# Optimization experiments

Hardware: AMD Instinct MI355X
Metric: run time of the kernel (lower is better)

The kernel has to match this reference:

```python
import jax, jax.numpy as jnp
import numpy as np

LECUN_A, LECUN_B = 1.7159, 0.666

def lecun_tanh(x):
    return LECUN_A * jnp.tanh(LECUN_B * x)

def setup_inputs() -> dict:
    key = jax.random.key(0)
    ks = jax.random.split(key, 16)
    B, T, D, H, BB, U, C = 128, 512, 1024, 512, 128, 32, 3
    def p(k, shape, fan_in):
        lim = 1.0 / np.sqrt(fan_in)
        return jax.random.uniform(k, shape, jnp.float32, -lim, lim)
    return {
        "x": jax.random.normal(ks[0], (B, T, D), jnp.float32),
        # vars[0], vars[1]: Linear(1024 -> 512)
        "W0": p(ks[1], (H, D), D), "b0": p(ks[2], (H,), D),
        # self.ltc CfC(512, 32): backbone Linear(512+32 -> 128), then ff1/ff2/time_a/time_b Linear(128 -> 32)
        "Wb": p(ks[3], (BB, H + U), H + U), "bb": p(ks[4], (BB,), H + U),
        "Wff1": p(ks[5], (U, BB), BB), "bff1": p(ks[6], (U,), BB),
        "Wff2": p(ks[7], (U, BB), BB), "bff2": p(ks[8], (U,), BB),
        "Wta": p(ks[9], (U, BB), BB), "bta": p(ks[10], (U,), BB),
        "Wtb": p(ks[11], (U, BB), BB), "btb": p(ks[12], (U,), BB),
        # vars[12], vars[13]: Linear(32 -> 3)
        "W2": p(ks[13], (C, U), U), "b2": p(ks[14], (C,), U),
    }

def reference(x, W0, b0, Wb, bb, Wff1, bff1, Wff2, bff2, Wta, bta, Wtb, btb, W2, b2):
    # x: [B, T, 1024] -> Linear -> GELU (dropout is identity in eval mode)
    h0 = jnp.einsum("btd,hd->bth", x, W0) + b0          # [B, T, 512]
    h0 = jax.nn.gelu(h0, approximate=False)
    B = x.shape[0]
    U = Wff1.shape[0]

    def step(h, xt):
        z = jnp.concatenate([xt, h], axis=-1)           # [B, 544]
        g = lecun_tanh(z @ Wb.T + bb)                   # backbone, [B, 128]
        ff1 = jnp.tanh(g @ Wff1.T + bff1)
        ff2 = jnp.tanh(g @ Wff2.T + bff2)
        t_a = g @ Wta.T + bta
        t_b = g @ Wtb.T + btb
        t_interp = jax.nn.sigmoid(t_a * 1.0 + t_b)      # ts = 1.0 per step
        h_new = ff1 * (1.0 - t_interp) + t_interp * ff2
        return h_new, h_new

    h_init = jnp.zeros((B, U), x.dtype)
    _, seq = jax.lax.scan(step, h_init, jnp.swapaxes(h0, 0, 1))  # [T, B, 32]
    seq = jnp.swapaxes(seq, 0, 1)                                # [B, T, 32]
    y = jax.nn.gelu(seq, approximate=False)
    logits = jnp.einsum("btu,cu->btc", y, W2) + b2               # [B, T, 3]
    pooled = jnp.max(logits, axis=1)                             # [B, 3]
    return jax.nn.softmax(pooled, axis=1)
```

## Files before the change

kernel.cpp:

```cpp
#include <hip/hip_runtime.h>
#include <hip/hip_bf16.h>
#include <cstdint>

typedef __bf16 bf16x8 __attribute__((ext_vector_type(8)));
typedef float  f32x4  __attribute__((ext_vector_type(4)));

__device__ __forceinline__ unsigned short f2bf(float f) {
    union { float f; uint32_t u; } v; v.f = f;
    uint32_t r = (v.u + 0x7FFFu + ((v.u >> 16) & 1u)) >> 16;
    return (unsigned short)r;
}

__device__ __forceinline__ float fast_tanh(float x) {
    x = fminf(10.f, fmaxf(-10.f, x));
    float e = __expf(2.f * x);
    return (e - 1.f) / (e + 1.f);
}

__device__ __forceinline__ float gelu_exact(float x) {
    return 0.5f * x * (1.0f + erff(x * 0.70710678118654752f));
}

__global__ __launch_bounds__(256) void convert_weights_kernel(
    const float* __restrict__ W0, const float* __restrict__ Wb,
    unsigned short* __restrict__ W0bf, unsigned short* __restrict__ Wbxbf)
{
    int i = blockIdx.x * 256 + threadIdx.x;
    if (i < 512 * 1024) W0bf[i] = f2bf(W0[i]);
    if (i < 128 * 512) {
        int n = i >> 9, k = i & 511;
        Wbxbf[i] = f2bf(Wb[n * 544 + k]);
    }
}

template <int NT, bool A_F32, bool GELU_OUT>
__global__ __launch_bounds__(256) void gemm_kernel(
    const void* __restrict__ Aptr, const unsigned short* __restrict__ B,
    const float* __restrict__ bias, void* __restrict__ Cptr,
    int M, int N, int K)
{
    __shared__ alignas(16) unsigned short Als[128 * 32];
    __shared__ alignas(16) unsigned short Bls[128 * 32];

    const int bid = blockIdx.x;
    const int nb = bid & (NT - 1);
    const int mb = bid / NT;
    const int m0 = mb * 128;
    const int n0 = nb * 128;

    const int t = threadIdx.x;
    const int w = t >> 6, l = t & 63;
    const int wr = w >> 1, wc = w & 1;
    const int lr = l & 15, lk = (l >> 4) * 8;

    f32x4 acc[4][4];
    const f32x4 zero = {0.f, 0.f, 0.f, 0.f};
#pragma unroll
    for (int i = 0; i < 4; ++i)
#pragma unroll
        for (int j = 0; j < 4; ++j) acc[i][j] = zero;

    for (int k0 = 0; k0 < K; k0 += 32) {
        if constexpr (A_F32) {
            const float* A = (const float*)Aptr;
#pragma unroll
            for (int p = 0; p < 4; ++p) {
                int r = p * 32 + (t >> 3);
                int kq = (t & 7) * 4;
                float4 v = *reinterpret_cast<const float4*>(
                    &A[(size_t)(m0 + r) * K + k0 + kq]);
                ushort4 o;
                o.x = f2bf(v.x); o.y = f2bf(v.y);
                o.z = f2bf(v.z); o.w = f2bf(v.w);
                *reinterpret_cast<ushort4*>(&Als[r * 32 + kq]) = o;
            }
        } else {
            const unsigned short* A = (const unsigned short*)Aptr;
#pragma unroll
            for (int p = 0; p < 2; ++p) {
                int r = p * 64 + (t >> 2);
                int kq = (t & 3) * 8;
                *reinterpret_cast<uint4*>(&Als[r * 32 + kq]) =
                    *reinterpret_cast<const uint4*>(&A[(size_t)(m0 + r) * K + k0 + kq]);
            }
        }
#pragma unroll
        for (int p = 0; p < 2; ++p) {
            int r = p * 64 + (t >> 2);
            int kq = (t & 3) * 8;
            *reinterpret_cast<uint4*>(&Bls[r * 32 + kq]) =
                *reinterpret_cast<const uint4*>(&B[(size_t)(n0 + r) * K + k0 + kq]);
        }
        __syncthreads();

        bf16x8 af[4], bfr[4];
#pragma unroll
        for (int i = 0; i < 4; ++i)
            af[i] = *reinterpret_cast<const bf16x8*>(&Als[(wr * 64 + i * 16 + lr) * 32 + lk]);
#pragma unroll
        for (int j = 0; j < 4; ++j)
            bfr[j] = *reinterpret_cast<const bf16x8*>(&Bls[(wc * 64 + j * 16 + lr) * 32 + lk]);
#pragma unroll
        for (int i = 0; i < 4; ++i)
#pragma unroll
            for (int j = 0; j < 4; ++j)
                acc[i][j] = __builtin_amdgcn_mfma_f32_16x16x32_bf16(
                    af[i], bfr[j], acc[i][j], 0, 0, 0);
        __syncthreads();
    }

#pragma unroll
    for (int i = 0; i < 4; ++i) {
#pragma unroll
        for (int j = 0; j < 4; ++j) {
            int col = n0 + wc * 64 + j * 16 + (l & 15);
            int rowb = m0 + wr * 64 + i * 16 + (l >> 4) * 4;
            float bv = bias[col];
#pragma unroll
            for (int p = 0; p < 4; ++p) {
                float v = acc[i][j][p] + bv;
                size_t idx = (size_t)(rowb + p) * N + col;
                if constexpr (GELU_OUT) {
                    ((unsigned short*)Cptr)[idx] = f2bf(gelu_exact(v));
                } else {
                    ((float*)Cptr)[idx] = v;
                }
            }
        }
    }
}

__global__ __launch_bounds__(512) void scan_kernel(
    const float* __restrict__ pre_g, const float* __restrict__ Wb,
    const float* __restrict__ Wff1, const float* __restrict__ bff1,
    const float* __restrict__ Wff2, const float* __restrict__ bff2,
    const float* __restrict__ Wta,  const float* __restrict__ bta,
    const float* __restrict__ Wtb,  const float* __restrict__ btb,
    float* __restrict__ seq)
{
    __shared__ alignas(16) float h_lds[32];
    __shared__ alignas(16) float g_lds[144];
    __shared__ alignas(16) float head_lds[128];

    const int tid = threadIdx.x;
    const int b = blockIdx.x;
    const int u = tid >> 2;
    const int q = tid & 3;

    float wbh[8];
#pragma unroll
    for (int j = 0; j < 8; ++j) wbh[j] = Wb[u * 544 + 512 + q * 8 + j];

    const int which = u >> 5;
    const int uu = u & 31;
    const float* Wh = (which == 0) ? Wff1 : (which == 1) ? Wff2 : (which == 2) ? Wta : Wtb;
    const float* bh = (which == 0) ? bff1 : (which == 1) ? bff2 : (which == 2) ? bta : btb;
    float whr[32];
#pragma unroll
    for (int j4 = 0; j4 < 8; ++j4) {
        float4 v = *reinterpret_cast<const float4*>(&Wh[uu * 128 + q * 32 + j4 * 4]);
        whr[j4 * 4 + 0] = v.x; whr[j4 * 4 + 1] = v.y;
        whr[j4 * 4 + 2] = v.z; whr[j4 * 4 + 3] = v.w;
    }
    const float hbias = bh[uu];

    if (tid < 32) h_lds[tid] = 0.0f;
    __syncthreads();

    const size_t base = (size_t)b * 512 * 128;
    const size_t sbase = (size_t)b * 512 * 32;
    float pg0 = pre_g[base + u];
    float pg1 = pre_g[base + 128 + u];

    for (int step = 0; step < 512; ++step) {
        float pg2 = 0.f;
        if (step + 2 < 512) pg2 = pre_g[base + (size_t)(step + 2) * 128 + u];

        float s = 0.f;
#pragma unroll
        for (int j2 = 0; j2 < 2; ++j2) {
            float4 hv = *reinterpret_cast<const float4*>(&h_lds[q * 8 + j2 * 4]);
            s = fmaf(wbh[j2 * 4 + 0], hv.x, s);
            s = fmaf(wbh[j2 * 4 + 1], hv.y, s);
            s = fmaf(wbh[j2 * 4 + 2], hv.z, s);
            s = fmaf(wbh[j2 * 4 + 3], hv.w, s);
        }
        s += __shfl_xor(s, 1);
        s += __shfl_xor(s, 2);
        float g = 1.7159f * fast_tanh(0.666f * (pg0 + s));
        if (q == 0) g_lds[u + ((u >> 5) << 2)] = g;
        __syncthreads();

        float d = 0.f;
        const float* gq = &g_lds[q * 36];
#pragma unroll
        for (int j4 = 0; j4 < 8; ++j4) {
            float4 gv = *reinterpret_cast<const float4*>(&gq[j4 * 4]);
            d = fmaf(whr[j4 * 4 + 0], gv.x, d);
            d = fmaf(whr[j4 * 4 + 1], gv.y, d);
            d = fmaf(whr[j4 * 4 + 2], gv.z, d);
            d = fmaf(whr[j4 * 4 + 3], gv.w, d);
        }
        d += __shfl_xor(d, 1);
        d += __shfl_xor(d, 2);
        d += hbias;
        if (u < 64) d = fast_tanh(d);
        if (q == 0) head_lds[u] = d;
        __syncthreads();

        if (tid < 32) {
            float ff1 = head_lds[tid], ff2 = head_lds[32 + tid];
            float ta = head_lds[64 + tid], tb = head_lds[96 + tid];
            float ti = 1.0f / (1.0f + __expf(-(ta + tb)));
            float hn = ff1 + ti * (ff2 - ff1);
            h_lds[tid] = hn;
            seq[sbase + (size_t)step * 32 + tid] = hn;
        }
        __syncthreads();

        pg0 = pg1; pg1 = pg2;
    }
}

__global__ __launch_bounds__(256) void final_kernel(
    const float* __restrict__ seq, const float* __restrict__ W2,
    const float* __restrict__ b2, float* __restrict__ out)
{
    const int b = blockIdx.x, tid = threadIdx.x;
    __shared__ float w2s[96];
    __shared__ float redbuf[12];
    if (tid < 96) w2s[tid] = W2[tid];
    __syncthreads();

    float m0 = -1e30f, m1 = -1e30f, m2 = -1e30f;
    for (int t = tid; t < 512; t += 256) {
        const float* row = &seq[(size_t)(b * 512 + t) * 32];
        float l0 = 0.f, l1 = 0.f, l2 = 0.f;
#pragma unroll
        for (int u4 = 0; u4 < 8; ++u4) {
            float4 v = *reinterpret_cast<const float4*>(&row[u4 * 4]);
            float xs[4] = {v.x, v.y, v.z, v.w};
#pragma unroll
            for (int e = 0; e < 4; ++e) {
                float y = gelu_exact(xs[e]);
                int uidx = u4 * 4 + e;
                l0 = fmaf(y, w2s[uidx], l0);
                l1 = fmaf(y, w2s[32 + uidx], l1);
                l2 = fmaf(y, w2s[64 + uidx], l2);
            }
        }
        m0 = fmaxf(m0, l0); m1 = fmaxf(m1, l1); m2 = fmaxf(m2, l2);
    }
#pragma unroll
    for (int off = 32; off; off >>= 1) {
        m0 = fmaxf(m0, __shfl_xor(m0, off));
        m1 = fmaxf(m1, __shfl_xor(m1, off));
        m2 = fmaxf(m2, __shfl_xor(m2, off));
    }
    if ((tid & 63) == 0) {
        int wv = tid >> 6;
        redbuf[wv * 3 + 0] = m0; redbuf[wv * 3 + 1] = m1; redbuf[wv * 3 + 2] = m2;
    }
    __syncthreads();
    if (tid == 0) {
        float a0 = -1e30f, a1 = -1e30f, a2 = -1e30f;
        for (int i = 0; i < 4; ++i) {
            a0 = fmaxf(a0, redbuf[i * 3 + 0]);
            a1 = fmaxf(a1, redbuf[i * 3 + 1]);
            a2 = fmaxf(a2, redbuf[i * 3 + 2]);
        }
        a0 += b2[0]; a1 += b2[1]; a2 += b2[2];
        float mm = fmaxf(a0, fmaxf(a1, a2));
        float e0 = expf(a0 - mm), e1 = expf(a1 - mm), e2 = expf(a2 - mm);
        float inv = 1.0f / (e0 + e1 + e2);
        out[b * 3 + 0] = e0 * inv;
        out[b * 3 + 1] = e1 * inv;
        out[b * 3 + 2] = e2 * inv;
    }
}

extern "C" void kernel_launch(void* const* d_in, const int* in_sizes, int n_in,
                              void* d_out, int out_size, void* d_ws, size_t ws_size,
                              hipStream_t stream)
{
    const float* x    = (const float*)d_in[0];
    const float* W0   = (const float*)d_in[1];
    const float* b0   = (const float*)d_in[2];
    const float* Wb   = (const float*)d_in[3];
    const float* bb   = (const float*)d_in[4];
    const float* Wff1 = (const float*)d_in[5];
    const float* bff1 = (const float*)d_in[6];
    const float* Wff2 = (const float*)d_in[7];
    const float* bff2 = (const float*)d_in[8];
    const float* Wta  = (const float*)d_in[9];
    const float* bta  = (const float*)d_in[10];
    const float* Wtb  = (const float*)d_in[11];
    const float* btb  = (const float*)d_in[12];
    const float* W2   = (const float*)d_in[13];
    const float* b2   = (const float*)d_in[14];

    char* ws = (char*)d_ws;
    unsigned short* h0bf  = (unsigned short*)(ws);
    float*          pre_g = (float*)(ws + 67108864);
    float*          seq   = (float*)(ws + 100663296);
    unsigned short* W0bf  = (unsigned short*)(ws + 109051904);
    unsigned short* Wbxbf = (unsigned short*)(ws + 110100480);
    (void)ws_size; (void)in_sizes; (void)n_in; (void)out_size;

    convert_weights_kernel<<<2048, 256, 0, stream>>>(W0, Wb, W0bf, Wbxbf);

    gemm_kernel<4, true, true><<<2048, 256, 0, stream>>>(
        (const void*)x, W0bf, b0, (void*)h0bf, 65536, 512, 1024);

    gemm_kernel<1, false, false><<<512, 256, 0, stream>>>(
        (const void*)h0bf, Wbxbf, bb, (void*)pre_g, 65536, 128, 512);

    scan_kernel<<<128, 512, 0, stream>>>(pre_g, Wb,
        Wff1, bff1, Wff2, bff2, Wta, bta, Wtb, btb, seq);

    final_kernel<<<128, 256, 0, stream>>>(seq, W2, b2, (float*)d_out);
}
```

Baseline: 948.9 us.

## Widen GEMM K-tile, restructure scan to two barriers per step, vectorize conversion

The GEMM K-tile grows from 32 to 64, which halves the number of barrier pairs per output tile at the cost of twice the shared memory. The scan kernel changes its head mapping so the four heads for one unit sit in the same 16 lanes. The gate combination is then done with shuffles, which drops the head_lds buffer and one __syncthreads per step. The scan also prefetches pre_g in chunks of 8 steps and splits its FMA chains into several independent accumulators, and weight conversion now uses float4 loads. The GEMM LDS layout, with a 64-element row stride, may cause more bank conflicts on the fragment reads.

```diff
diff --git a/kernel.cpp b/kernel.cpp
--- a/kernel.cpp
+++ b/kernel.cpp
@@ -26,10 +26,18 @@
     unsigned short* __restrict__ W0bf, unsigned short* __restrict__ Wbxbf)
 {
     int i = blockIdx.x * 256 + threadIdx.x;
-    if (i < 512 * 1024) W0bf[i] = f2bf(W0[i]);
-    if (i < 128 * 512) {
-        int n = i >> 9, k = i & 511;
-        Wbxbf[i] = f2bf(Wb[n * 544 + k]);
+    if (i < 131072) {
+        float4 v = reinterpret_cast<const float4*>(W0)[i];
+        ushort4 o;
+        o.x = f2bf(v.x); o.y = f2bf(v.y); o.z = f2bf(v.z); o.w = f2bf(v.w);
+        reinterpret_cast<ushort4*>(W0bf)[i] = o;
+    }
+    if (i < 16384) {
+        int n = i >> 7, k4 = i & 127;
+        float4 v = *reinterpret_cast<const float4*>(&Wb[n * 544 + k4 * 4]);
+        ushort4 o;
+        o.x = f2bf(v.x); o.y = f2bf(v.y); o.z = f2bf(v.z); o.w = f2bf(v.w);
+        reinterpret_cast<ushort4*>(Wbxbf)[i] = o;
     }
 }
 
@@ -39,8 +47,8 @@
     const float* __restrict__ bias, void* __restrict__ Cptr,
     int M, int N, int K)
 {
-    __shared__ alignas(16) unsigned short Als[128 * 32];
-    __shared__ alignas(16) unsigned short Bls[128 * 32];
+    __shared__ alignas(16) unsigned short Als[128 * 64];
+    __shared__ alignas(16) unsigned short Bls[128 * 64];
 
     const int bid = blockIdx.x;
     const int nb = bid & (NT - 1);
@@ -60,52 +68,57 @@
 #pragma unroll
         for (int j = 0; j < 4; ++j) acc[i][j] = zero;
 
-    for (int k0 = 0; k0 < K; k0 += 32) {
+    for (int k0 = 0; k0 < K; k0 += 64) {
         if constexpr (A_F32) {
             const float* A = (const float*)Aptr;
 #pragma unroll
-            for (int p = 0; p < 4; ++p) {
-                int r = p * 32 + (t >> 3);
-                int kq = (t & 7) * 4;
+            for (int p = 0; p < 8; ++p) {
+                int r = p * 16 + (t >> 4);
+                int kq = (t & 15) * 4;
                 float4 v = *reinterpret_cast<const float4*>(
                     &A[(size_t)(m0 + r) * K + k0 + kq]);
                 ushort4 o;
                 o.x = f2bf(v.x); o.y = f2bf(v.y);
                 o.z = f2bf(v.z); o.w = f2bf(v.w);
-                *reinterpret_cast<ushort4*>(&Als[r * 32 + kq]) = o;
+                *reinterpret_cast<ushort4*>(&Als[r * 64 + kq]) = o;
             }
         } else {
             const unsigned short* A = (const unsigned short*)Aptr;
 #pragma unroll
-            for (int p = 0; p < 2; ++p) {
-                int r = p * 64 + (t >> 2);
-                int kq = (t & 3) * 8;
-                *reinterpret_cast<uint4*>(&Als[r * 32 + kq]) =
-                    *reinterpret_cast<const uint4*>(&A[(size_t)(m0 + r) * K + k0 + kq]);
-            }
-        }
-#pragma unroll
-        for (int p = 0; p < 2; ++p) {
-            int r = p * 64 + (t >> 2);
-            int kq = (t & 3) * 8;
-            *reinterpret_cast<uint4*>(&Bls[r * 32 + kq]) =
-                *reinterpret_cast<const uint4*>(&B[(size_t)(n0 + r) * K + k0 + kq]);
+            for (int p = 0; p < 4; ++p) {
+                int idx = p * 256 + t;
+                int r = idx >> 3, c = (idx & 7) * 8;
+                *reinterpret_cast<uint4*>(&Als[r * 64 + c]) =
+                    *reinterpret_cast<const uint4*>(&A[(size_t)(m0 + r) * K + k0 + c]);
+            }
+        }
+#pragma unroll
+        for (int p = 0; p < 4; ++p) {
+            int idx = p * 256 + t;
+            int r = idx >> 3, c = (idx & 7) * 8;
+            *reinterpret_cast<uint4*>(&Bls[r * 64 + c]) =
+                *reinterpret_cast<const uint4*>(&B[(size_t)(n0 + r) * K + k0 + c]);
         }
         __syncthreads();
 
-        bf16x8 af[4], bfr[4];
-#pragma unroll
-        for (int i = 0; i < 4; ++i)
-            af[i] = *reinterpret_cast<const bf16x8*>(&Als[(wr * 64 + i * 16 + lr) * 32 + lk]);
-#pragma unroll
-        for (int j = 0; j < 4; ++j)
-            bfr[j] = *reinterpret_cast<const bf16x8*>(&Bls[(wc * 64 + j * 16 + lr) * 32 + lk]);
-#pragma unroll
-        for (int i = 0; i < 4; ++i)
+#pragma unroll
+        for (int kk = 0; kk < 64; kk += 32) {
+            bf16x8 af[4], bfr[4];
+#pragma unroll
+            for (int i = 0; i < 4; ++i)
+                af[i] = *reinterpret_cast<const bf16x8*>(
+                    &Als[(wr * 64 + i * 16 + lr) * 64 + kk + lk]);
 #pragma unroll
             for (int j = 0; j < 4; ++j)
-                acc[i][j] = __builtin_amdgcn_mfma_f32_16x16x32_bf16(
-                    af[i], bfr[j], acc[i][j], 0, 0, 0);
+                bfr[j] = *reinterpret_cast<const bf16x8*>(
+                    &Bls[(wc * 64 + j * 16 + lr) * 64 + kk + lk]);
+#pragma unroll
+            for (int i = 0; i < 4; ++i)
+#pragma unroll
+                for (int j = 0; j < 4; ++j)
+                    acc[i][j] = __builtin_amdgcn_mfma_f32_16x16x32_bf16(
+                        af[i], bfr[j], acc[i][j], 0, 0, 0);
+        }
         __syncthreads();
     }
 
@@ -140,85 +153,104 @@
 {
     __shared__ alignas(16) float h_lds[32];
     __shared__ alignas(16) float g_lds[144];
-    __shared__ alignas(16) float head_lds[128];
 
     const int tid = threadIdx.x;
     const int b = blockIdx.x;
-    const int u = tid >> 2;
-    const int q = tid & 3;
-
+
+    const int u = tid >> 2, q = tid & 3;
     float wbh[8];
 #pragma unroll
-    for (int j = 0; j < 8; ++j) wbh[j] = Wb[u * 544 + 512 + q * 8 + j];
-
-    const int which = u >> 5;
-    const int uu = u & 31;
-    const float* Wh = (which == 0) ? Wff1 : (which == 1) ? Wff2 : (which == 2) ? Wta : Wtb;
-    const float* bh = (which == 0) ? bff1 : (which == 1) ? bff2 : (which == 2) ? bta : btb;
+    for (int i = 0; i < 8; ++i) wbh[i] = Wb[u * 544 + 512 + q * 8 + i];
+
+    const int j = tid >> 4;
+    const int hh = (tid >> 2) & 3;
+    const int q2 = tid & 3;
+    const float* Wh = (hh == 0) ? Wff1 : (hh == 1) ? Wff2 : (hh == 2) ? Wta : Wtb;
+    const float* bh = (hh == 0) ? bff1 : (hh == 1) ? bff2 : (hh == 2) ? bta : btb;
     float whr[32];
 #pragma unroll
-    for (int j4 = 0; j4 < 8; ++j4) {
-        float4 v = *reinterpret_cast<const float4*>(&Wh[uu * 128 + q * 32 + j4 * 4]);
-        whr[j4 * 4 + 0] = v.x; whr[j4 * 4 + 1] = v.y;
-        whr[j4 * 4 + 2] = v.z; whr[j4 * 4 + 3] = v.w;
-    }
-    const float hbias = bh[uu];
+    for (int k4 = 0; k4 < 8; ++k4) {
+        float4 v = *reinterpret_cast<const float4*>(&Wh[j * 128 + q2 * 32 + k4 * 4]);
+        whr[k4 * 4 + 0] = v.x; whr[k4 * 4 + 1] = v.y;
+        whr[k4 * 4 + 2] = v.z; whr[k4 * 4 + 3] = v.w;
+    }
+    const float hbias = bh[j];
 
     if (tid < 32) h_lds[tid] = 0.0f;
     __syncthreads();
 
-    const size_t base = (size_t)b * 512 * 128;
-    const size_t sbase = (size_t)b * 512 * 32;
-    float pg0 = pre_g[base + u];
-    float pg1 = pre_g[base + 128 + u];
-
-    for (int step = 0; step < 512; ++step) {
-        float pg2 = 0.f;
-        if (step + 2 < 512) pg2 = pre_g[base + (size_t)(step + 2) * 128 + u];
-
-        float s = 0.f;
-#pragma unroll
-        for (int j2 = 0; j2 < 2; ++j2) {
-            float4 hv = *reinterpret_cast<const float4*>(&h_lds[q * 8 + j2 * 4]);
-            s = fmaf(wbh[j2 * 4 + 0], hv.x, s);
-            s = fmaf(wbh[j2 * 4 + 1], hv.y, s);
-            s = fmaf(wbh[j2 * 4 + 2], hv.z, s);
-            s = fmaf(wbh[j2 * 4 + 3], hv.w, s);
-        }
-        s += __shfl_xor(s, 1);
-        s += __shfl_xor(s, 2);
-        float g = 1.7159f * fast_tanh(0.666f * (pg0 + s));
-        if (q == 0) g_lds[u + ((u >> 5) << 2)] = g;
-        __syncthreads();
-
-        float d = 0.f;
-        const float* gq = &g_lds[q * 36];
-#pragma unroll
-        for (int j4 = 0; j4 < 8; ++j4) {
-            float4 gv = *reinterpret_cast<const float4*>(&gq[j4 * 4]);
-            d = fmaf(whr[j4 * 4 + 0], gv.x, d);
-            d = fmaf(whr[j4 * 4 + 1], gv.y, d);
-            d = fmaf(whr[j4 * 4 + 2], gv.z, d);
-            d = fmaf(whr[j4 * 4 + 3], gv.w, d);
-        }
-        d += __shfl_xor(d, 1);
-        d += __shfl_xor(d, 2);
-        d += hbias;
-        if (u < 64) d = fast_tanh(d);
-        if (q == 0) head_lds[u] = d;
-        __syncthreads();
-
-        if (tid < 32) {
-            float ff1 = head_lds[tid], ff2 = head_lds[32 + tid];
-            float ta = head_lds[64 + tid], tb = head_lds[96 + tid];
-            float ti = 1.0f / (1.0f + __expf(-(ta + tb)));
-            float hn = ff1 + ti * (ff2 - ff1);
-            h_lds[tid] = hn;
-            seq[sbase + (size_t)step * 32 + tid] = hn;
-        }
-        __syncthreads();
-
-        pg0 = pg1; pg1 = pg2;
+    const float* pgp = pre_g + (size_t)b * 512 * 128 + u;
+    float* seqp = seq + (size_t)b * 512 * 32;
+
+    float pgbuf[8], pgnext[8];
+#pragma unroll
+    for (int i = 0; i < 8; ++i) pgbuf[i] = pgp[(size_t)i * 128];
+
+    for (int c = 0; c < 64; ++c) {
+        if (c < 63) {
+#pragma unroll
+            for (int i = 0; i < 8; ++i)
+                pgnext[i] = pgp[(size_t)((c + 1) * 8 + i) * 128];
+        }
+#pragma unroll
+        for (int s8 = 0; s8 < 8; ++s8) {
+            const int step = c * 8 + s8;
+            float4 hv0 = *reinterpret_cast<const float4*>(&h_lds[q * 8]);
+            float4 hv1 = *reinterpret_cast<const float4*>(&h_lds[q * 8 + 4]);
+            float s0 = wbh[0] * hv0.x, s1 = wbh[1] * hv0.y;
+            s0 = fmaf(wbh[2], hv0.z, s0); s1 = fmaf(wbh[3], hv0.w, s1);
+            s0 = fmaf(wbh[4], hv1.x, s0); s1 = fmaf(wbh[5], hv1.y, s1);
+            s0 = fmaf(wbh[6], hv1.z, s0); s1 = fmaf(wbh[7], hv1.w, s1);
+            float s = s0 + s1;
+            s += __shfl_xor(s, 1);
+            s += __shfl_xor(s, 2);
+            float g = 1.7159f * fast_tanh(0.666f * (pgbuf[s8] + s));
+            if (q == 0) g_lds[u + ((u >> 5) << 2)] = g;
+            __syncthreads();
+
+            const float* gq = &g_lds[q2 * 36];
+            float d0 = 0.f, d1 = 0.f, d2 = 0.f, d3 = 0.f;
+#pragma unroll
+            for (int k4 = 0; k4 < 8; k4 += 4) {
+                float4 ga = *reinterpret_cast<const float4*>(&gq[k4 * 4]);
+                float4 gb = *reinterpret_cast<const float4*>(&gq[k4 * 4 + 4]);
+                float4 gc = *reinterpret_cast<const float4*>(&gq[k4 * 4 + 8]);
+                float4 gd = *reinterpret_cast<const float4*>(&gq[k4 * 4 + 12]);
+                d0 = fmaf(whr[k4 * 4 + 0], ga.x, d0);
+                d1 = fmaf(whr[k4 * 4 + 1], ga.y, d1);
+                d2 = fmaf(whr[k4 * 4 + 2], ga.z, d2);
+                d3 = fmaf(whr[k4 * 4 + 3], ga.w, d3);
+                d0 = fmaf(whr[k4 * 4 + 4], gb.x, d0);
+                d1 = fmaf(whr[k4 * 4 + 5], gb.y, d1);
+                d2 = fmaf(whr[k4 * 4 + 6], gb.z, d2);
+                d3 = fmaf(whr[k4 * 4 + 7], gb.w, d3);
+                d0 = fmaf(whr[k4 * 4 + 8], gc.x, d0);
+                d1 = fmaf(whr[k4 * 4 + 9], gc.y, d1);
+                d2 = fmaf(whr[k4 * 4 + 10], gc.z, d2);
+                d3 = fmaf(whr[k4 * 4 + 11], gc.w, d3);
+                d0 = fmaf(whr[k4 * 4 + 12], gd.x, d0);
+                d1 = fmaf(whr[k4 * 4 + 13], gd.y, d1);
+                d2 = fmaf(whr[k4 * 4 + 14], gd.z, d2);
+                d3 = fmaf(whr[k4 * 4 + 15], gd.w, d3);
+            }
+            float d = (d0 + d1) + (d2 + d3);
+            d += __shfl_xor(d, 1);
+            d += __shfl_xor(d, 2);
+            d += hbias;
+            if (hh < 2) d = fast_tanh(d);
+            float vff2 = __shfl_xor(d, 4);
+            float vta  = __shfl_xor(d, 8);
+            float vtb  = __shfl_xor(d, 12);
+            float ti = 1.0f / (1.0f + __expf(-(vta + vtb)));
+            float hn = fmaf(ti, vff2 - d, d);
+            if ((tid & 15) == 0) {
+                h_lds[j] = hn;
+                seqp[(size_t)step * 32 + j] = hn;
+            }
+            __syncthreads();
+        }
+#pragma unroll
+        for (int i = 0; i < 8; ++i) pgbuf[i] = pgnext[i];
     }
 }
 
@@ -307,7 +339,7 @@
     unsigned short* Wbxbf = (unsigned short*)(ws + 110100480);
     (void)ws_size; (void)in_sizes; (void)n_in; (void)out_size;
 
-    convert_weights_kernel<<<2048, 256, 0, stream>>>(W0, Wb, W0bf, Wbxbf);
+    convert_weights_kernel<<<512, 256, 0, stream>>>(W0, Wb, W0bf, Wbxbf);
 
     gemm_kernel<4, true, true><<<2048, 256, 0, stream>>>(
         (const void*)x, W0bf, b0, (void*)h0bf, 65536, 512, 1024);
```

Result: faster. 907.9 us (-4.3%).
